# Kernel tuning notes

Measured on AMD Instinct MI355X. Metric: run time of the kernel, lower is better.

The kernel has to match this reference:

```python
import jax, jax.numpy as jnp
import numpy as np

B, T, D = 8, 4096, 1024


def setup_inputs() -> dict:
    key = jax.random.key(0)
    k1, k2 = jax.random.split(key)
    x = jax.random.normal(k1, (B, T, D), dtype=jnp.float32)
    lengths = jax.random.randint(k2, (B,), 0, T, dtype=jnp.int64)
    return {"x": x, "lengths": lengths}


def reference(x, lengths):
    # x: [B, T, D]; lengths: [B]
    # Original torch code materializes a [B,T,T,D] tensor via
    # (tril * pairwise_padding_mask)[..., None] * gelu(x)[:, None] and sums over
    # the source axis. Algebraically:
    #   out[b,i] = x[b,i] + m[b,i] * sum_{j<=i} m[b,j] * gelu(x[b,j])
    # where m[b,t] = (t < lengths[b]). This is a masked causal prefix sum.
    t = x.shape[1]
    valid = (jnp.arange(t)[None, :] < lengths[:, None]).astype(x.dtype)  # [B,T]
    g = jax.nn.gelu(x, approximate=False) * valid[:, :, None]           # [B,T,D]
    prefix = jnp.cumsum(g, axis=1)                                      # [B,T,D]
    return x + valid[:, :, None] * prefix
```

## Files before the change

### kernel.cpp

```cpp
#include <hip/hip_runtime.h>
#include <math.h>

#define BB 8
#define TT 4096
#define DD 1024
#define NC 256
#define CT (TT / NC)
#define D4 (DD / 4)

typedef float vfloat4 __attribute__((ext_vector_type(4)));

__device__ __forceinline__ float gelu_fast(float v) {
    const float x  = v * 0.70710678118654752f;
    const float ax = fabsf(x);
    const float t  = __builtin_amdgcn_rcpf(fmaf(0.3275911f, ax, 1.0f));
    float p = fmaf(1.061405429f, t, -1.453152027f);
    p = fmaf(p, t, 1.421413741f);
    p = fmaf(p, t, -0.284496736f);
    p = fmaf(p, t, 0.254829592f);
    const float e  = __expf(-ax * ax);
    const float er = fmaf(-p * t, e, 1.0f);
    const float erf_x = copysignf(er, x);
    return 0.5f * v * (1.0f + erf_x);
}

__device__ __forceinline__ void gelu_acc(float4& s, const float4 v) {
    s.x += gelu_fast(v.x);
    s.y += gelu_fast(v.y);
    s.z += gelu_fast(v.z);
    s.w += gelu_fast(v.w);
}

__device__ __forceinline__ void f4_acc(float4& s, const float4 a) {
    s.x += a.x; s.y += a.y; s.z += a.z; s.w += a.w;
}

__global__ __launch_bounds__(256)
void k_partial(const float* __restrict__ x, const int* __restrict__ lengths,
               float* __restrict__ ws) {
    const int c  = blockIdx.x;
    const int b  = blockIdx.y;
    const int d4 = threadIdx.x;
    const int len = lengths[b];
    const int t0 = c * CT;
    if (t0 >= len) return;
    const int t1 = min(t0 + CT, len);

    const float4* __restrict__ xp = (const float4*)(x + (size_t)b * TT * DD);
    float4 s = make_float4(0.f, 0.f, 0.f, 0.f);
    #pragma unroll 4
    for (int t = t0; t < t1; ++t) {
        float4 v = xp[(size_t)t * D4 + d4];
        gelu_acc(s, v);
    }
    ((float4*)ws)[((size_t)b * NC + c) * D4 + d4] = s;
}

__global__ __launch_bounds__(256)
void k_apply(const float* __restrict__ x, const int* __restrict__ lengths,
             const float* __restrict__ ws, float* __restrict__ out) {
    const int c  = blockIdx.x;
    const int b  = blockIdx.y;
    const int d4 = threadIdx.x;
    const int len = lengths[b];
    const int t0 = c * CT;
    const int tv = min(t0 + CT, len);

    const float4* __restrict__ xp = (const float4*)(x + (size_t)b * TT * DD);
    vfloat4* __restrict__ op = (vfloat4*)(out + (size_t)b * TT * DD);

    int t = t0;
    if (t0 < len) {
        float4 p0 = make_float4(0.f, 0.f, 0.f, 0.f);
        float4 p1 = make_float4(0.f, 0.f, 0.f, 0.f);
        const float4* __restrict__ aggp =
            (const float4*)ws + (size_t)b * NC * D4 + d4;
        int cc = 0;
        #pragma unroll 4
        for (; cc + 1 < c; cc += 2) {
            float4 a0 = aggp[(size_t)cc * D4];
            float4 a1 = aggp[(size_t)(cc + 1) * D4];
            f4_acc(p0, a0);
            f4_acc(p1, a1);
        }
        if (cc < c) f4_acc(p0, aggp[(size_t)cc * D4]);
        float4 pre = make_float4(p0.x + p1.x, p0.y + p1.y,
                                 p0.z + p1.z, p0.w + p1.w);

        #pragma unroll 4
        for (; t < tv; ++t) {
            float4 v = xp[(size_t)t * D4 + d4];
            gelu_acc(pre, v);
            vfloat4 o = {v.x + pre.x, v.y + pre.y, v.z + pre.z, v.w + pre.w};
            __builtin_nontemporal_store(o, &op[(size_t)t * D4 + d4]);
        }
    }
    #pragma unroll 4
    for (; t < t0 + CT; ++t) {
        float4 v = xp[(size_t)t * D4 + d4];
        vfloat4 o = {v.x, v.y, v.z, v.w};
        __builtin_nontemporal_store(o, &op[(size_t)t * D4 + d4]);
    }
}

extern "C" void kernel_launch(void* const* d_in, const int* in_sizes, int n_in,
                              void* d_out, int out_size, void* d_ws, size_t ws_size,
                              hipStream_t stream) {
    const float* x       = (const float*)d_in[0];
    const int*   lengths = (const int*)d_in[1];
    float*       out     = (float*)d_out;
    float*       ws      = (float*)d_ws;

    dim3 blk(256, 1, 1);
    dim3 g1(NC, BB, 1);
    hipLaunchKernelGGL(k_partial, g1, blk, 0, stream, x, lengths, ws);
    hipLaunchKernelGGL(k_apply,   g1, blk, 0, stream, x, lengths, ws, out);
}
```

Baseline: 256.0 us.

## Store per-pair running sums in partial pass and preload apply chunk into registers

The partial kernel now runs one block per pair of chunks and writes a running sum at each chunk boundary, so odd slots hold two-chunk totals. The apply kernel therefore reads about half as many workspace entries to build each chunk's prefix. The apply kernel also loads all 16 rows of its chunk into registers up front, so global loads overlap the prefix reduction, and the main loop is fully unrolled with a per-row validity branch. The cost is fewer blocks in the partial pass and higher register pressure in the apply kernel, which may lower occupancy.

```diff
diff --git a/kernel.cpp b/kernel.cpp
--- a/kernel.cpp
+++ b/kernel.cpp
@@ -7,6 +7,10 @@
 #define NC 256
 #define CT (TT / NC)
 #define D4 (DD / 4)
+#define NCS 128
+#define CPS 2
+#define CTS (CT * CPS)
+
 
 typedef float vfloat4 __attribute__((ext_vector_type(4)));
 
@@ -38,22 +42,29 @@
 __global__ __launch_bounds__(256)
 void k_partial(const float* __restrict__ x, const int* __restrict__ lengths,
                float* __restrict__ ws) {
-    const int c  = blockIdx.x;
+    const int s  = blockIdx.x;
     const int b  = blockIdx.y;
     const int d4 = threadIdx.x;
     const int len = lengths[b];
-    const int t0 = c * CT;
-    if (t0 >= len) return;
-    const int t1 = min(t0 + CT, len);
+    const int t0s = s * CTS;
+    if (t0s >= len) return;
 
     const float4* __restrict__ xp = (const float4*)(x + (size_t)b * TT * DD);
-    float4 s = make_float4(0.f, 0.f, 0.f, 0.f);
-    #pragma unroll 4
-    for (int t = t0; t < t1; ++t) {
-        float4 v = xp[(size_t)t * D4 + d4];
-        gelu_acc(s, v);
+    float4* __restrict__ aggw =
+        (float4*)ws + ((size_t)b * NC + (size_t)s * CPS) * D4 + d4;
+
+    float4 run = make_float4(0.f, 0.f, 0.f, 0.f);
+    #pragma unroll
+    for (int j = 0; j < CPS; ++j) {
+        const int tj0 = t0s + j * CT;
+        const int tj1 = min(tj0 + CT, len);
+        #pragma unroll 4
+        for (int t = tj0; t < tj1; ++t) {
+            float4 v = xp[(size_t)t * D4 + d4];
+            gelu_acc(run, v);
+        }
+        aggw[(size_t)j * D4] = run;
     }
-    ((float4*)ws)[((size_t)b * NC + c) * D4 + d4] = s;
 }
 
 __global__ __launch_bounds__(256)
@@ -69,36 +80,39 @@
     const float4* __restrict__ xp = (const float4*)(x + (size_t)b * TT * DD);
     vfloat4* __restrict__ op = (vfloat4*)(out + (size_t)b * TT * DD);
 
-    int t = t0;
-    if (t0 < len) {
-        float4 p0 = make_float4(0.f, 0.f, 0.f, 0.f);
-        float4 p1 = make_float4(0.f, 0.f, 0.f, 0.f);
+    float4 r[CT];
+    #pragma unroll
+    for (int i = 0; i < CT; ++i)
+        r[i] = xp[(size_t)(t0 + i) * D4 + d4];
+
+    float4 pre = make_float4(0.f, 0.f, 0.f, 0.f);
+    if (t0 < len && c > 0) {
         const float4* __restrict__ aggp =
             (const float4*)ws + (size_t)b * NC * D4 + d4;
-        int cc = 0;
+        const int sc = c >> 1;
+        float4 p1 = make_float4(0.f, 0.f, 0.f, 0.f);
+        int ss = 0;
         #pragma unroll 4
-        for (; cc + 1 < c; cc += 2) {
-            float4 a0 = aggp[(size_t)cc * D4];
-            float4 a1 = aggp[(size_t)(cc + 1) * D4];
-            f4_acc(p0, a0);
-            f4_acc(p1, a1);
+        for (; ss + 1 < sc; ss += 2) {
+            f4_acc(pre, aggp[(size_t)(2 * ss + 1) * D4]);
+            f4_acc(p1,  aggp[(size_t)(2 * ss + 3) * D4]);
         }
-        if (cc < c) f4_acc(p0, aggp[(size_t)cc * D4]);
-        float4 pre = make_float4(p0.x + p1.x, p0.y + p1.y,
-                                 p0.z + p1.z, p0.w + p1.w);
+        if (ss < sc) f4_acc(pre, aggp[(size_t)(2 * ss + 1) * D4]);
+        if (c & 1)   f4_acc(pre, aggp[(size_t)(c - 1) * D4]);
+        f4_acc(pre, p1);
+    }
 
-        #pragma unroll 4
-        for (; t < tv; ++t) {
-            float4 v = xp[(size_t)t * D4 + d4];
+    #pragma unroll
+    for (int i = 0; i < CT; ++i) {
+        const int t = t0 + i;
+        const float4 v = r[i];
+        vfloat4 o;
+        if (t < tv) {
             gelu_acc(pre, v);
-            vfloat4 o = {v.x + pre.x, v.y + pre.y, v.z + pre.z, v.w + pre.w};
-            __builtin_nontemporal_store(o, &op[(size_t)t * D4 + d4]);
+            o = {v.x + pre.x, v.y + pre.y, v.z + pre.z, v.w + pre.w};
+        } else {
+            o = {v.x, v.y, v.z, v.w};
         }
-    }
-    #pragma unroll 4
-    for (; t < t0 + CT; ++t) {
-        float4 v = xp[(size_t)t * D4 + d4];
-        vfloat4 o = {v.x, v.y, v.z, v.w};
         __builtin_nontemporal_store(o, &op[(size_t)t * D4 + d4]);
     }
 }
@@ -112,7 +126,9 @@
     float*       ws      = (float*)d_ws;
 
     dim3 blk(256, 1, 1);
-    dim3 g1(NC, BB, 1);
+    dim3 g1(NCS, BB, 1);
     hipLaunchKernelGGL(k_partial, g1, blk, 0, stream, x, lengths, ws);
-    hipLaunchKernelGGL(k_apply,   g1, blk, 0, stream, x, lengths, ws, out);
+
+    dim3 g2(NC, BB, 1);
+    hipLaunchKernelGGL(k_apply, g2, blk, 0, stream, x, lengths, ws, out);
 }
```

Measured after the change: 243.6 us. -4.8%, faster.
